# Kernel tuning notes

Hardware: AMD Instinct MI355X
Metric: run time of the kernel (lower is better)

Reference implementation:

```python
import jax, jax.numpy as jnp
import numpy as np

NN, D, H = 100000, 300, 1024   # nodes, embedding dim, hidden dim
NG, NS = 50000, 25000          # global vocab, sense vocab
B, T = 8, 128                  # batch, sequence length (state carried across all B*T steps)


def setup_inputs() -> dict:
    key = jax.random.key(0)
    ks = jax.random.split(key, 24)
    s = lambda i, shape: (jax.random.normal(ks[i], shape, jnp.float32) * 0.02)
    return {
        "x_idx": jax.random.randint(ks[0], (B, T), 0, NN),
        "X": jax.random.normal(ks[1], (NN, D), jnp.float32) * 0.1,
        "W_z_1": s(2, (D, H)), "U_z_1": s(3, (H, H)),
        "W_r_1": s(4, (D, H)), "U_r_1": s(5, (H, H)),
        "W_1": s(6, (D, H)), "b_W_1": jnp.zeros((H,), jnp.float32),
        "U_1": s(7, (H, H)), "b_U_1": jnp.zeros((H,), jnp.float32),
        "W_z_2": s(8, (H, H)), "U_z_2": s(9, (H, H)),
        "W_r_2": s(10, (H, H)), "U_r_2": s(11, (H, H)),
        "W_2": s(12, (H, H)), "b_W_2": jnp.zeros((H,), jnp.float32),
        "U_2": s(13, (H, H)), "b_U_2": jnp.zeros((H,), jnp.float32),
        "W_g": s(14, (H, NG)), "b_g": jnp.zeros((NG,), jnp.float32),
        "W_s": s(15, (H, NS)), "b_s": jnp.zeros((NS,), jnp.float32),
    }


def reference(x_idx, X, W_z_1, U_z_1, W_r_1, U_r_1, W_1, b_W_1, U_1, b_U_1,
              W_z_2, U_z_2, W_r_2, U_r_2, W_2, b_W_2, U_2, b_U_2,
              W_g, b_g, W_s, b_s):
    # The original loops over every sample of every sequence, carrying memory_h1/h2
    # across the whole batch; only X[x_indices[0]] feeds the GRU (the GAT-projected
    # neighbours are computed but never used). Dropout in eval mode = identity.
    idx = x_idx.reshape(-1)          # [S] flattened step order (seq-major per sample)
    emb = X[idx]                     # [S, D] currentword embeddings

    def step(carry, e):
        h1, h2 = carry
        z1 = jax.nn.sigmoid(e @ W_z_1 + h1 @ U_z_1)
        r1 = jax.nn.sigmoid(e @ W_r_1 + h1 @ U_r_1)
        ht1 = jnp.tanh((e @ W_1 + b_W_1) + ((r1 * h1) @ U_1 + b_U_1))
        h1n = z1 * ht1 + (1.0 - z1) * h1
        z2 = jax.nn.sigmoid(h1n @ W_z_2 + h2 @ U_z_2)
        r2 = jax.nn.sigmoid(h1n @ W_r_2 + h2 @ U_r_2)
        ht2 = jnp.tanh((h1n @ W_2 + b_W_2) + ((r2 * h2) @ U_2 + b_U_2))
        h2n = z2 * ht2 + (1.0 - z2) * h2
        return (h1n, h2n), h2n

    h0 = jnp.zeros((H,), emb.dtype)
    _, hs = jax.lax.scan(step, (h0, h0), emb)        # hs: [S, H]
    logp_g = jax.nn.log_softmax(hs @ W_g + b_g, axis=-1)   # [S, NG]
    logp_s = jax.nn.log_softmax(hs @ W_s + b_s, axis=-1)   # [S, NS]
    return logp_g, logp_s
```

## Files before the change

### kernel.cpp

```cpp
#include <hip/hip_runtime.h>

typedef __attribute__((ext_vector_type(4))) float f32x4;
typedef __attribute__((ext_vector_type(8))) __bf16 bf16x8;
typedef __attribute__((ext_vector_type(4))) unsigned short u16x4;
typedef unsigned long long ull;

#define GPAD 40
#define KEEPF(x) asm volatile("" : "+v"(x))
#define PHYS(i) ((i) + (((i) >> 6) << 2))

__device__ ull g_R[32 * 1024];
__device__ ull g_h1s[1025 * 1024];
__device__ float g_ExW[1024 * 3072];
__device__ float g_hs2[1024 * 1024];

#define H1R  0
#define RH1R (8 * 1024)
#define H2R  (16 * 1024)
#define RH2R (24 * 1024)

__device__ __forceinline__ unsigned short f2bf(float x) {
  unsigned u = __builtin_bit_cast(unsigned, x);
  u += 0x7FFFu + ((u >> 16) & 1u);
  return (unsigned short)(u >> 16);
}
__device__ __forceinline__ ull packtv(unsigned tag, float v) {
  return ((ull)tag << 32) | (ull)__builtin_bit_cast(unsigned, v);
}
__device__ __forceinline__ ull aload(const ull* p) {
  return __hip_atomic_load(p, __ATOMIC_RELAXED, __HIP_MEMORY_SCOPE_AGENT);
}
__device__ __forceinline__ void astore(ull* p, ull v) {
  __hip_atomic_store(p, v, __ATOMIC_RELAXED, __HIP_MEMORY_SCOPE_AGENT);
}
__device__ __forceinline__ float lo32(ull v) {
  return __builtin_bit_cast(float, (unsigned)v);
}

__global__ __launch_bounds__(256, 1) void fused_scan(
    const float* __restrict__ ExW,
    const float* __restrict__ Uz1, const float* __restrict__ Ur1,
    const float* __restrict__ Uw1, const float* __restrict__ bU1,
    const float* __restrict__ Wz2, const float* __restrict__ Wr2,
    const float* __restrict__ Ww2,
    const float* __restrict__ Uz2, const float* __restrict__ Ur2,
    const float* __restrict__ Uw2,
    const float* __restrict__ bW2, const float* __restrict__ bU2,
    float* __restrict__ hs2)
{
  const int tid = threadIdx.x;
  const int wv = tid >> 6, inw = tid & 63;
  __shared__ __align__(16) float h_s[1088];
  __shared__ __align__(16) float rh_s[1088];
  __shared__ __align__(16) float x_s[1088];

  if (blockIdx.x < 64) {
    const int g = blockIdx.x;
    const int rep = g & 7;
    const int c2 = inw >> 4, q = inw & 15;
    const int j = g * 16 + wv * 4 + c2;
    const int prj = g * 16 + wv * 4 + (inw >> 4);
    const bool pub = (inw & 15) < 8;
    float uz[64], ur[64], uw[64];
#pragma unroll
    for (int i = 0; i < 64; ++i) uz[i] = Uz1[(size_t)(q * 64 + i) * 1024 + j];
#pragma unroll
    for (int i = 0; i < 64; ++i) ur[i] = Ur1[(size_t)(q * 64 + i) * 1024 + j];
#pragma unroll
    for (int i = 0; i < 64; ++i) uw[i] = Uw1[(size_t)(q * 64 + i) * 1024 + j];
#pragma unroll
    for (int i = 0; i < 64; ++i) { KEEPF(uz[i]); KEEPF(ur[i]); KEEPF(uw[i]); }
    const float bu = bU1[j];

    float xz = 0.f, xr = 0.f, xw = 0.f;
    if (q == 0) { xz = ExW[j]; xr = ExW[1024 + j]; xw = ExW[2048 + j]; }

    float zreg = 0.f, hold = 0.f;
    for (int s = 0; s < 1024; ++s) {
      {
        const ull* sl = g_R + H1R + (size_t)rep * 1024 + tid * 4;
        ull a0, a1, a2, a3;
        for (;;) {
          a0 = aload(sl); a1 = aload(sl + 1); a2 = aload(sl + 2); a3 = aload(sl + 3);
          unsigned bad = ((unsigned)(a0 >> 32) ^ (unsigned)s) | ((unsigned)(a1 >> 32) ^ (unsigned)s) |
                         ((unsigned)(a2 >> 32) ^ (unsigned)s) | ((unsigned)(a3 >> 32) ^ (unsigned)s);
          if (bad == 0u) break;
          __builtin_amdgcn_s_sleep(1);
        }
        f32x4 v; v.x = lo32(a0); v.y = lo32(a1); v.z = lo32(a2); v.w = lo32(a3);
        *(f32x4*)&h_s[PHYS(tid * 4)] = v;
      }
      __syncthreads();
      if (q == 0) hold = h_s[PHYS(j)];
      float ar_ = 0.f;
      {
        const float* hp = h_s + q * 68;
#pragma unroll
        for (int i2 = 0; i2 < 16; ++i2) {
          f32x4 hv = *(const f32x4*)(hp + i2 * 4);
          ar_ = fmaf(ur[i2 * 4 + 0], hv.x, ar_); ar_ = fmaf(ur[i2 * 4 + 1], hv.y, ar_);
          ar_ = fmaf(ur[i2 * 4 + 2], hv.z, ar_); ar_ = fmaf(ur[i2 * 4 + 3], hv.w, ar_);
        }
      }
      ar_ += __shfl_xor(ar_, 1, 64); ar_ += __shfl_xor(ar_, 2, 64);
      ar_ += __shfl_xor(ar_, 4, 64); ar_ += __shfl_xor(ar_, 8, 64);
      float rhv = 0.f;
      if (q == 0) {
        float r = 1.f / (1.f + __expf(-(ar_ + xr)));
        rhv = r * hold;
      }
      {
        float pvv = __shfl(rhv, inw & 48, 64);
        ull pk = packtv((unsigned)(s + 1), pvv);
        if (pub) astore(g_R + RH1R + (size_t)(inw & 15) * 1024 + prj, pk);
      }
      float az_ = 0.f;
      {
        const float* hp = h_s + q * 68;
#pragma unroll
        for (int i2 = 0; i2 < 16; ++i2) {
          f32x4 hv = *(const f32x4*)(hp + i2 * 4);
          az_ = fmaf(uz[i2 * 4 + 0], hv.x, az_); az_ = fmaf(uz[i2 * 4 + 1], hv.y, az_);
          az_ = fmaf(uz[i2 * 4 + 2], hv.z, az_); az_ = fmaf(uz[i2 * 4 + 3], hv.w, az_);
        }
      }
      az_ += __shfl_xor(az_, 1, 64); az_ += __shfl_xor(az_, 2, 64);
      az_ += __shfl_xor(az_, 4, 64); az_ += __shfl_xor(az_, 8, 64);
      if (q == 0) zreg = 1.f / (1.f + __expf(-(az_ + xz)));
      {
        const ull* sl = g_R + RH1R + (size_t)rep * 1024 + tid * 4;
        ull a0, a1, a2, a3;
        const unsigned tg = (unsigned)(s + 1);
        for (;;) {
          a0 = aload(sl); a1 = aload(sl + 1); a2 = aload(sl + 2); a3 = aload(sl + 3);
          unsigned bad = ((unsigned)(a0 >> 32) ^ tg) | ((unsigned)(a1 >> 32) ^ tg) |
                         ((unsigned)(a2 >> 32) ^ tg) | ((unsigned)(a3 >> 32) ^ tg);
          if (bad == 0u) break;
          __builtin_amdgcn_s_sleep(1);
        }
        f32x4 v; v.x = lo32(a0); v.y = lo32(a1); v.z = lo32(a2); v.w = lo32(a3);
        *(f32x4*)&rh_s[PHYS(tid * 4)] = v;
      }
      __syncthreads();
      float aw_ = 0.f;
      {
        const float* rp = rh_s + q * 68;
#pragma unroll
        for (int i2 = 0; i2 < 16; ++i2) {
          f32x4 rv = *(const f32x4*)(rp + i2 * 4);
          aw_ = fmaf(uw[i2 * 4 + 0], rv.x, aw_); aw_ = fmaf(uw[i2 * 4 + 1], rv.y, aw_);
          aw_ = fmaf(uw[i2 * 4 + 2], rv.z, aw_); aw_ = fmaf(uw[i2 * 4 + 3], rv.w, aw_);
        }
      }
      aw_ += __shfl_xor(aw_, 1, 64); aw_ += __shfl_xor(aw_, 2, 64);
      aw_ += __shfl_xor(aw_, 4, 64); aw_ += __shfl_xor(aw_, 8, 64);
      float hn = 0.f;
      if (q == 0) {
        float ht = tanhf(aw_ + xw + bu);
        hn = zreg * ht + (1.f - zreg) * hold;
      }
      {
        float pvv = __shfl(hn, inw & 48, 64);
        ull pk = packtv((unsigned)(s + 1), pvv);
        if (pub) astore(g_R + H1R + (size_t)(inw & 15) * 1024 + prj, pk);
        if (q == 0) astore(&g_h1s[(size_t)(s + 1) * 1024 + j], pk);
      }
      float nxz = 0.f, nxr = 0.f, nxw = 0.f;
      if (q == 0 && s < 1023) {
        nxz = ExW[(s + 1) * 3072 + j];
        nxr = ExW[(s + 1) * 3072 + 1024 + j];
        nxw = ExW[(s + 1) * 3072 + 2048 + j];
      }
      xz = nxz; xr = nxr; xw = nxw;
    }
  } else {
    const int g = blockIdx.x - 64;
    const int rep = g & 7;
    const int c2 = inw >> 5, q = inw & 31;
    const int j = g * 8 + wv * 2 + c2;
    const int sb = q * 32 + ((q >> 1) << 2);
    const int prj = g * 8 + wv * 2 + (inw >> 5);
    const bool pub = (inw & 31) < 8;
    float uz[32], ur[32], uw[32], wz[32], wr[32], ww[32];
#pragma unroll
    for (int i = 0; i < 32; ++i) uz[i] = Uz2[(size_t)(q * 32 + i) * 1024 + j];
#pragma unroll
    for (int i = 0; i < 32; ++i) ur[i] = Ur2[(size_t)(q * 32 + i) * 1024 + j];
#pragma unroll
    for (int i = 0; i < 32; ++i) uw[i] = Uw2[(size_t)(q * 32 + i) * 1024 + j];
#pragma unroll
    for (int i = 0; i < 32; ++i) wz[i] = Wz2[(size_t)(q * 32 + i) * 1024 + j];
#pragma unroll
    for (int i = 0; i < 32; ++i) wr[i] = Wr2[(size_t)(q * 32 + i) * 1024 + j];
#pragma unroll
    for (int i = 0; i < 32; ++i) ww[i] = Ww2[(size_t)(q * 32 + i) * 1024 + j];
#pragma unroll
    for (int i = 0; i < 32; ++i) {
      KEEPF(uz[i]); KEEPF(ur[i]); KEEPF(uw[i]);
      KEEPF(wz[i]); KEEPF(wr[i]); KEEPF(ww[i]);
    }
    const float bu = bW2[j] + bU2[j];

    float zreg = 0.f, hold = 0.f;
    for (int s = 0; s < 1024; ++s) {
      {
        const ull* sh = g_R + H2R + (size_t)rep * 1024 + tid * 4;
        const ull* sx = g_h1s + (size_t)(s + 1) * 1024 + tid * 4;
        ull a0, a1, a2, a3, b0, b1, b2, b3;
        const unsigned tg = (unsigned)(s + 1);
        for (;;) {
          a0 = aload(sh); a1 = aload(sh + 1); a2 = aload(sh + 2); a3 = aload(sh + 3);
          b0 = aload(sx); b1 = aload(sx + 1); b2 = aload(sx + 2); b3 = aload(sx + 3);
          unsigned bad = ((unsigned)(a0 >> 32) ^ (unsigned)s) | ((unsigned)(a1 >> 32) ^ (unsigned)s) |
                         ((unsigned)(a2 >> 32) ^ (unsigned)s) | ((unsigned)(a3 >> 32) ^ (unsigned)s) |
                         ((unsigned)(b0 >> 32) ^ tg) | ((unsigned)(b1 >> 32) ^ tg) |
                         ((unsigned)(b2 >> 32) ^ tg) | ((unsigned)(b3 >> 32) ^ tg);
          if (bad == 0u) break;
          __builtin_amdgcn_s_sleep(2);
        }
        f32x4 v; v.x = lo32(a0); v.y = lo32(a1); v.z = lo32(a2); v.w = lo32(a3);
        *(f32x4*)&h_s[PHYS(tid * 4)] = v;
        f32x4 u4; u4.x = lo32(b0); u4.y = lo32(b1); u4.z = lo32(b2); u4.w = lo32(b3);
        *(f32x4*)&x_s[PHYS(tid * 4)] = u4;
      }
      __syncthreads();
      if (q == 0) hold = h_s[PHYS(j)];
      float ar_ = 0.f;
      {
        const float* hp = h_s + sb;
        const float* xp = x_s + sb;
#pragma unroll
        for (int i2 = 0; i2 < 8; ++i2) {
          f32x4 hv = *(const f32x4*)(hp + i2 * 4);
          f32x4 xv = *(const f32x4*)(xp + i2 * 4);
          ar_ = fmaf(ur[i2 * 4 + 0], hv.x, ar_); ar_ = fmaf(ur[i2 * 4 + 1], hv.y, ar_);
          ar_ = fmaf(ur[i2 * 4 + 2], hv.z, ar_); ar_ = fmaf(ur[i2 * 4 + 3], hv.w, ar_);
          ar_ = fmaf(wr[i2 * 4 + 0], xv.x, ar_); ar_ = fmaf(wr[i2 * 4 + 1], xv.y, ar_);
          ar_ = fmaf(wr[i2 * 4 + 2], xv.z, ar_); ar_ = fmaf(wr[i2 * 4 + 3], xv.w, ar_);
        }
      }
      ar_ += __shfl_xor(ar_, 1, 64); ar_ += __shfl_xor(ar_, 2, 64);
      ar_ += __shfl_xor(ar_, 4, 64); ar_ += __shfl_xor(ar_, 8, 64);
      ar_ += __shfl_xor(ar_, 16, 64);
      float rhv = 0.f;
      if (q == 0) {
        float r = 1.f / (1.f + __expf(-ar_));
        rhv = r * hold;
      }
      {
        float pvv = __shfl(rhv, inw & 32, 64);
        ull pk = packtv((unsigned)(s + 1), pvv);
        if (pub) astore(g_R + RH2R + (size_t)(inw & 31) * 1024 + prj, pk);
      }
      float az_ = 0.f;
      {
        const float* hp = h_s + sb;
        const float* xp = x_s + sb;
#pragma unroll
        for (int i2 = 0; i2 < 8; ++i2) {
          f32x4 hv = *(const f32x4*)(hp + i2 * 4);
          f32x4 xv = *(const f32x4*)(xp + i2 * 4);
          az_ = fmaf(uz[i2 * 4 + 0], hv.x, az_); az_ = fmaf(uz[i2 * 4 + 1], hv.y, az_);
          az_ = fmaf(uz[i2 * 4 + 2], hv.z, az_); az_ = fmaf(uz[i2 * 4 + 3], hv.w, az_);
          az_ = fmaf(wz[i2 * 4 + 0], xv.x, az_); az_ = fmaf(wz[i2 * 4 + 1], xv.y, az_);
          az_ = fmaf(wz[i2 * 4 + 2], xv.z, az_); az_ = fmaf(wz[i2 * 4 + 3], xv.w, az_);
        }
      }
      az_ += __shfl_xor(az_, 1, 64); az_ += __shfl_xor(az_, 2, 64);
      az_ += __shfl_xor(az_, 4, 64); az_ += __shfl_xor(az_, 8, 64);
      az_ += __shfl_xor(az_, 16, 64);
      if (q == 0) zreg = 1.f / (1.f + __expf(-az_));
      {
        const ull* sl = g_R + RH2R + (size_t)rep * 1024 + tid * 4;
        ull a0, a1, a2, a3;
        const unsigned tg = (unsigned)(s + 1);
        for (;;) {
          a0 = aload(sl); a1 = aload(sl + 1); a2 = aload(sl + 2); a3 = aload(sl + 3);
          unsigned bad = ((unsigned)(a0 >> 32) ^ tg) | ((unsigned)(a1 >> 32) ^ tg) |
                         ((unsigned)(a2 >> 32) ^ tg) | ((unsigned)(a3 >> 32) ^ tg);
          if (bad == 0u) break;
          __builtin_amdgcn_s_sleep(1);
        }
        f32x4 v; v.x = lo32(a0); v.y = lo32(a1); v.z = lo32(a2); v.w = lo32(a3);
        *(f32x4*)&rh_s[PHYS(tid * 4)] = v;
      }
      __syncthreads();
      float aw_ = 0.f;
      {
        const float* rp = rh_s + sb;
        const float* xp = x_s + sb;
#pragma unroll
        for (int i2 = 0; i2 < 8; ++i2) {
          f32x4 rv = *(const f32x4*)(rp + i2 * 4);
          f32x4 xv = *(const f32x4*)(xp + i2 * 4);
          aw_ = fmaf(uw[i2 * 4 + 0], rv.x, aw_); aw_ = fmaf(uw[i2 * 4 + 1], rv.y, aw_);
          aw_ = fmaf(uw[i2 * 4 + 2], rv.z, aw_); aw_ = fmaf(uw[i2 * 4 + 3], rv.w, aw_);
          aw_ = fmaf(ww[i2 * 4 + 0], xv.x, aw_); aw_ = fmaf(ww[i2 * 4 + 1], xv.y, aw_);
          aw_ = fmaf(ww[i2 * 4 + 2], xv.z, aw_); aw_ = fmaf(ww[i2 * 4 + 3], xv.w, aw_);
        }
      }
      aw_ += __shfl_xor(aw_, 1, 64); aw_ += __shfl_xor(aw_, 2, 64);
      aw_ += __shfl_xor(aw_, 4, 64); aw_ += __shfl_xor(aw_, 8, 64);
      aw_ += __shfl_xor(aw_, 16, 64);
      float hn = 0.f;
      if (q == 0) {
        float ht = tanhf(aw_ + bu);
        hn = zreg * ht + (1.f - zreg) * hold;
        hs2[(size_t)s * 1024 + j] = hn;
      }
      {
        float pvv = __shfl(hn, inw & 32, 64);
        ull pk = packtv((unsigned)(s + 1), pvv);
        if (pub) astore(g_R + H2R + (size_t)(inw & 31) * 1024 + prj, pk);
      }
    }
  }
}

__global__ __launch_bounds__(256, 1) void gemm_mfma(
    const float* __restrict__ A, const int* __restrict__ gidx, int lda,
    const float* __restrict__ B, int ldb,
    const float* __restrict__ bias,
    float* __restrict__ C, int ldc, int N, int K)
{
  __shared__ unsigned short As[128 * GPAD];
  __shared__ unsigned short Bs[128 * GPAD];
  const int tid = threadIdx.x;
  const int lane = tid & 63;
  const int wv = tid >> 6;
  const int wm = wv >> 1, wn = wv & 1;
  const int mbase = blockIdx.y * 128, nbase = blockIdx.x * 128;

  f32x4 acc[4][4];
#pragma unroll
  for (int i = 0; i < 4; ++i)
#pragma unroll
    for (int qq = 0; qq < 4; ++qq) acc[i][qq] = (f32x4){0.f, 0.f, 0.f, 0.f};

  const int ar = tid >> 1, ak = (tid & 1) * 16;
  const float* Arow;
  {
    int m = mbase + ar;
    long long gr = gidx ? (long long)gidx[m] : (long long)m;
    Arow = A + (size_t)gr * (size_t)lda;
  }
  const int bn = (tid >> 3) * 4;
  const int bk = (tid & 7) * 4;
  const bool nedge = (nbase + 128 > N);

  const int ksteps = (K + 31) >> 5;
  for (int ks = 0; ks < ksteps; ++ks) {
    const int k0 = ks << 5;
    __syncthreads();
    {
      float v[16];
      const int kg = k0 + ak;
      if (kg + 16 <= K) {
#pragma unroll
        for (int qq = 0; qq < 4; ++qq) {
          f32x4 t = *(const f32x4*)(Arow + kg + qq * 4);
          v[qq * 4 + 0] = t.x; v[qq * 4 + 1] = t.y; v[qq * 4 + 2] = t.z; v[qq * 4 + 3] = t.w;
        }
      } else {
#pragma unroll
        for (int i = 0; i < 16; ++i) v[i] = (kg + i < K) ? Arow[kg + i] : 0.f;
      }
#pragma unroll
      for (int qq = 0; qq < 4; ++qq) {
        u16x4 wq;
        wq.x = f2bf(v[qq * 4 + 0]); wq.y = f2bf(v[qq * 4 + 1]);
        wq.z = f2bf(v[qq * 4 + 2]); wq.w = f2bf(v[qq * 4 + 3]);
        *(u16x4*)&As[ar * GPAD + ak + qq * 4] = wq;
      }
    }
    {
      float bv[4][4];
#pragma unroll
      for (int kk = 0; kk < 4; ++kk) {
        int kglob = k0 + bk + kk;
        if (kglob < K) {
          if (!nedge) {
            f32x4 t = *(const f32x4*)(B + (size_t)kglob * (size_t)ldb + nbase + bn);
            bv[kk][0] = t.x; bv[kk][1] = t.y; bv[kk][2] = t.z; bv[kk][3] = t.w;
          } else {
#pragma unroll
            for (int nn = 0; nn < 4; ++nn) {
              int n = nbase + bn + nn;
              bv[kk][nn] = (n < N) ? B[(size_t)kglob * (size_t)ldb + n] : 0.f;
            }
          }
        } else {
          bv[kk][0] = bv[kk][1] = bv[kk][2] = bv[kk][3] = 0.f;
        }
      }
#pragma unroll
      for (int nn = 0; nn < 4; ++nn) {
        u16x4 wq;
        wq.x = f2bf(bv[0][nn]); wq.y = f2bf(bv[1][nn]);
        wq.z = f2bf(bv[2][nn]); wq.w = f2bf(bv[3][nn]);
        *(u16x4*)&Bs[(bn + nn) * GPAD + bk] = wq;
      }
    }
    __syncthreads();
    bf16x8 af[4], bfr[4];
    const int fr = lane & 15, fk = (lane >> 4) * 8;
#pragma unroll
    for (int mf = 0; mf < 4; ++mf)
      af[mf] = *(const bf16x8*)&As[(wm * 64 + mf * 16 + fr) * GPAD + fk];
#pragma unroll
    for (int nf = 0; nf < 4; ++nf)
      bfr[nf] = *(const bf16x8*)&Bs[(wn * 64 + nf * 16 + fr) * GPAD + fk];
#pragma unroll
    for (int mf = 0; mf < 4; ++mf)
#pragma unroll
      for (int nf = 0; nf < 4; ++nf)
        acc[mf][nf] = __builtin_amdgcn_mfma_f32_16x16x32_bf16(af[mf], bfr[nf], acc[mf][nf], 0, 0, 0);
  }
  const int fr = lane & 15, fq = lane >> 4;
#pragma unroll
  for (int nf = 0; nf < 4; ++nf) {
    int col = nbase + wn * 64 + nf * 16 + fr;
    if (col < N) {
      float bb = bias ? bias[col] : 0.f;
#pragma unroll
      for (int mf = 0; mf < 4; ++mf) {
        int row0 = mbase + wm * 64 + mf * 16 + fq * 4;
#pragma unroll
        for (int r = 0; r < 4; ++r)
          C[(size_t)(row0 + r) * (size_t)ldc + col] = acc[mf][nf][r] + bb;
      }
    }
  }
}

__global__ __launch_bounds__(256, 1) void logsoftmax_kernel(float* __restrict__ out) {
  const int row = blockIdx.x;
  float* p; int len;
  if (row < 1024) { p = out + (size_t)row * 50000u; len = 50000; }
  else            { p = out + 51200000ull + (size_t)(row - 1024) * 25000u; len = 25000; }
  const int tid = threadIdx.x;
  __shared__ float mred[4], sred[4];

  float m = -3.4e38f;
  for (int i = tid * 4; i < len; i += 1024) {
    f32x4 v = *(const f32x4*)(p + i);
    m = fmaxf(m, fmaxf(fmaxf(v.x, v.y), fmaxf(v.z, v.w)));
  }
#pragma unroll
  for (int off = 32; off >= 1; off >>= 1) m = fmaxf(m, __shfl_xor(m, off, 64));
  if ((tid & 63) == 0) mred[tid >> 6] = m;
  __syncthreads();
  m = fmaxf(fmaxf(mred[0], mred[1]), fmaxf(mred[2], mred[3]));

  float ssum = 0.f;
  for (int i = tid * 4; i < len; i += 1024) {
    f32x4 v = *(const f32x4*)(p + i);
    ssum += __expf(v.x - m) + __expf(v.y - m) + __expf(v.z - m) + __expf(v.w - m);
  }
#pragma unroll
  for (int off = 32; off >= 1; off >>= 1) ssum += __shfl_xor(ssum, off, 64);
  if ((tid & 63) == 0) sred[tid >> 6] = ssum;
  __syncthreads();
  const float lse = m + logf(sred[0] + sred[1] + sred[2] + sred[3]);

  for (int i = tid * 4; i < len; i += 1024) {
    f32x4 v = *(const f32x4*)(p + i);
    v.x -= lse; v.y -= lse; v.z -= lse; v.w -= lse;
    *(f32x4*)(p + i) = v;
  }
}

extern "C" void kernel_launch(void* const* d_in, const int* in_sizes, int n_in,
                              void* d_out, int out_size, void* d_ws, size_t ws_size,
                              hipStream_t stream) {
  (void)in_sizes; (void)n_in; (void)out_size; (void)d_ws; (void)ws_size;
  const int*   x_idx = (const int*)  d_in[0];
  const float* X     = (const float*)d_in[1];
  const float* W_z_1 = (const float*)d_in[2];
  const float* U_z_1 = (const float*)d_in[3];
  const float* W_r_1 = (const float*)d_in[4];
  const float* U_r_1 = (const float*)d_in[5];
  const float* W_1   = (const float*)d_in[6];
  const float* b_W_1 = (const float*)d_in[7];
  const float* U_1   = (const float*)d_in[8];
  const float* b_U_1 = (const float*)d_in[9];
  const float* W_z_2 = (const float*)d_in[10];
  const float* U_z_2 = (const float*)d_in[11];
  const float* W_r_2 = (const float*)d_in[12];
  const float* U_r_2 = (const float*)d_in[13];
  const float* W_2   = (const float*)d_in[14];
  const float* b_W_2 = (const float*)d_in[15];
  const float* U_2   = (const float*)d_in[16];
  const float* b_U_2 = (const float*)d_in[17];
  const float* W_g   = (const float*)d_in[18];
  const float* b_g   = (const float*)d_in[19];
  const float* W_s   = (const float*)d_in[20];
  const float* b_s   = (const float*)d_in[21];
  float* out = (float*)d_out;

  float *ExW, *hs2;
  ull *R, *h1s;
  hipGetSymbolAddress((void**)&ExW, HIP_SYMBOL(g_ExW));
  hipGetSymbolAddress((void**)&hs2, HIP_SYMBOL(g_hs2));
  hipGetSymbolAddress((void**)&R, HIP_SYMBOL(g_R));
  hipGetSymbolAddress((void**)&h1s, HIP_SYMBOL(g_h1s));

  const dim3 blk(256);

  hipMemsetAsync(R, 0, 32ull * 1024 * sizeof(ull), stream);
  hipMemsetAsync(h1s, 0, 1025ull * 1024 * sizeof(ull), stream);

  gemm_mfma<<<dim3(8, 8), blk, 0, stream>>>(X, x_idx, 300, W_z_1, 1024, nullptr, ExW + 0,    3072, 1024, 300);
  gemm_mfma<<<dim3(8, 8), blk, 0, stream>>>(X, x_idx, 300, W_r_1, 1024, nullptr, ExW + 1024, 3072, 1024, 300);
  gemm_mfma<<<dim3(8, 8), blk, 0, stream>>>(X, x_idx, 300, W_1,   1024, b_W_1,   ExW + 2048, 3072, 1024, 300);

  fused_scan<<<dim3(192), blk, 0, stream>>>(
      ExW, U_z_1, U_r_1, U_1, b_U_1,
      W_z_2, W_r_2, W_2, U_z_2, U_r_2, U_2, b_W_2, b_U_2, hs2);

  gemm_mfma<<<dim3(391, 8), blk, 0, stream>>>(hs2, nullptr, 1024, W_g, 50000, b_g, out,              50000, 50000, 1024);
  gemm_mfma<<<dim3(196, 8), blk, 0, stream>>>(hs2, nullptr, 1024, W_s, 25000, b_s, out + 51200000ll, 25000, 25000, 1024);
  logsoftmax_kernel<<<dim3(2048), blk, 0, stream>>>(out);
}
```

Baseline: 6.432 ms.

## Fuse output projection GEMMs into scan kernel to overlap with recurrence

```diff
diff --git a/kernel.cpp b/kernel.cpp
--- a/kernel.cpp
+++ b/kernel.cpp
@@ -11,8 +11,8 @@
 
 __device__ ull g_R[32 * 1024];
 __device__ ull g_h1s[1025 * 1024];
+__device__ ull g_h2s[1024 * 1024];
 __device__ float g_ExW[1024 * 3072];
-__device__ float g_hs2[1024 * 1024];
 
 #define H1R  0
 #define RH1R (8 * 1024)
@@ -35,6 +35,10 @@
 }
 __device__ __forceinline__ float lo32(ull v) {
   return __builtin_bit_cast(float, (unsigned)v);
+}
+__device__ __forceinline__ unsigned tagbad4(ull a0, ull a1, ull a2, ull a3, unsigned tg) {
+  return ((unsigned)(a0 >> 32) ^ tg) | ((unsigned)(a1 >> 32) ^ tg) |
+         ((unsigned)(a2 >> 32) ^ tg) | ((unsigned)(a3 >> 32) ^ tg);
 }
 
 __global__ __launch_bounds__(256, 1) void fused_scan(
@@ -46,15 +50,17 @@
     const float* __restrict__ Uz2, const float* __restrict__ Ur2,
     const float* __restrict__ Uw2,
     const float* __restrict__ bW2, const float* __restrict__ bU2,
-    float* __restrict__ hs2)
+    const float* __restrict__ Wg, const float* __restrict__ bg,
+    const float* __restrict__ Ws, const float* __restrict__ bs,
+    float* __restrict__ out)
 {
   const int tid = threadIdx.x;
   const int wv = tid >> 6, inw = tid & 63;
-  __shared__ __align__(16) float h_s[1088];
-  __shared__ __align__(16) float rh_s[1088];
-  __shared__ __align__(16) float x_s[1088];
+  __shared__ __align__(16) char smem[20480];
 
   if (blockIdx.x < 64) {
+    float* h_s = (float*)smem;
+    float* rh_s = h_s + 1088;
     const int g = blockIdx.x;
     const int rep = g & 7;
     const int c2 = inw >> 4, q = inw & 15;
@@ -82,9 +88,7 @@
         ull a0, a1, a2, a3;
         for (;;) {
           a0 = aload(sl); a1 = aload(sl + 1); a2 = aload(sl + 2); a3 = aload(sl + 3);
-          unsigned bad = ((unsigned)(a0 >> 32) ^ (unsigned)s) | ((unsigned)(a1 >> 32) ^ (unsigned)s) |
-                         ((unsigned)(a2 >> 32) ^ (unsigned)s) | ((unsigned)(a3 >> 32) ^ (unsigned)s);
-          if (bad == 0u) break;
+          if (!tagbad4(a0, a1, a2, a3, (unsigned)s)) break;
           __builtin_amdgcn_s_sleep(1);
         }
         f32x4 v; v.x = lo32(a0); v.y = lo32(a1); v.z = lo32(a2); v.w = lo32(a3);
@@ -133,9 +137,7 @@
         const unsigned tg = (unsigned)(s + 1);
         for (;;) {
           a0 = aload(sl); a1 = aload(sl + 1); a2 = aload(sl + 2); a3 = aload(sl + 3);
-          unsigned bad = ((unsigned)(a0 >> 32) ^ tg) | ((unsigned)(a1 >> 32) ^ tg) |
-                         ((unsigned)(a2 >> 32) ^ tg) | ((unsigned)(a3 >> 32) ^ tg);
-          if (bad == 0u) break;
+          if (!tagbad4(a0, a1, a2, a3, tg)) break;
           __builtin_amdgcn_s_sleep(1);
         }
         f32x4 v; v.x = lo32(a0); v.y = lo32(a1); v.z = lo32(a2); v.w = lo32(a3);
@@ -173,7 +175,10 @@
       }
       xz = nxz; xr = nxr; xw = nxw;
     }
-  } else {
+  } else if (blockIdx.x < 192) {
+    float* h_s = (float*)smem;
+    float* rh_s = h_s + 1088;
+    float* x_s = rh_s + 1088;
     const int g = blockIdx.x - 64;
     const int rep = g & 7;
     const int c2 = inw >> 5, q = inw & 31;
@@ -211,10 +216,7 @@
         for (;;) {
           a0 = aload(sh); a1 = aload(sh + 1); a2 = aload(sh + 2); a3 = aload(sh + 3);
           b0 = aload(sx); b1 = aload(sx + 1); b2 = aload(sx + 2); b3 = aload(sx + 3);
-          unsigned bad = ((unsigned)(a0 >> 32) ^ (unsigned)s) | ((unsigned)(a1 >> 32) ^ (unsigned)s) |
-                         ((unsigned)(a2 >> 32) ^ (unsigned)s) | ((unsigned)(a3 >> 32) ^ (unsigned)s) |
-                         ((unsigned)(b0 >> 32) ^ tg) | ((unsigned)(b1 >> 32) ^ tg) |
-                         ((unsigned)(b2 >> 32) ^ tg) | ((unsigned)(b3 >> 32) ^ tg);
+          unsigned bad = tagbad4(a0, a1, a2, a3, (unsigned)s) | tagbad4(b0, b1, b2, b3, tg);
           if (bad == 0u) break;
           __builtin_amdgcn_s_sleep(2);
         }
@@ -276,9 +278,7 @@
         const unsigned tg = (unsigned)(s + 1);
         for (;;) {
           a0 = aload(sl); a1 = aload(sl + 1); a2 = aload(sl + 2); a3 = aload(sl + 3);
-          unsigned bad = ((unsigned)(a0 >> 32) ^ tg) | ((unsigned)(a1 >> 32) ^ tg) |
-                         ((unsigned)(a2 >> 32) ^ tg) | ((unsigned)(a3 >> 32) ^ tg);
-          if (bad == 0u) break;
+          if (!tagbad4(a0, a1, a2, a3, tg)) break;
           __builtin_amdgcn_s_sleep(1);
         }
         f32x4 v; v.x = lo32(a0); v.y = lo32(a1); v.z = lo32(a2); v.w = lo32(a3);
@@ -306,13 +306,134 @@
       if (q == 0) {
         float ht = tanhf(aw_ + bu);
         hn = zreg * ht + (1.f - zreg) * hold;
-        hs2[(size_t)s * 1024 + j] = hn;
+        astore(&g_h2s[(size_t)s * 1024 + j], packtv((unsigned)(s + 1), hn));
       }
       {
         float pvv = __shfl(hn, inw & 32, 64);
         ull pk = packtv((unsigned)(s + 1), pvv);
         if (pub) astore(g_R + H2R + (size_t)(inw & 31) * 1024 + prj, pk);
       }
+    }
+  } else {
+    unsigned short* As = (unsigned short*)smem;
+    unsigned short* Bs = As + 128 * GPAD;
+    const int wid = blockIdx.x - 192;
+    const int lane = tid & 63;
+    const int wm = wv >> 1, wn = wv & 1;
+    const int ar = tid >> 1, ak = (tid & 1) * 16;
+    const int bn = (tid >> 3) * 4, bk = (tid & 7) * 4;
+    const int TILES = 587 * 8;
+
+    for (int t5 = wid; t5 < TILES; t5 += 64) {
+      const int rt = t5 / 587, u = t5 % 587;
+      const float* B; const float* bias; float* C; int N; int ct;
+      if (u < 391) { B = Wg; bias = bg; C = out; N = 50000; ct = u; }
+      else         { B = Ws; bias = bs; C = out + 51200000ll; N = 25000; ct = u - 391; }
+      const int mbase = rt * 128, nbase = ct * 128;
+      const bool nedge = (nbase + 128 > N);
+
+      {
+        const ull* gp = g_h2s + (size_t)(mbase + 127) * 1024 + tid * 4;
+        const unsigned tg = (unsigned)(mbase + 128);
+        for (;;) {
+          ull a0 = aload(gp), a1 = aload(gp + 1), a2 = aload(gp + 2), a3 = aload(gp + 3);
+          if (!tagbad4(a0, a1, a2, a3, tg)) break;
+          __builtin_amdgcn_s_sleep(32);
+        }
+      }
+      __syncthreads();
+
+      f32x4 acc[4][4];
+#pragma unroll
+      for (int i = 0; i < 4; ++i)
+#pragma unroll
+        for (int qq = 0; qq < 4; ++qq) acc[i][qq] = (f32x4){0.f, 0.f, 0.f, 0.f};
+
+      for (int ks = 0; ks < 32; ++ks) {
+        const int k0 = ks << 5;
+        __syncthreads();
+        {
+          const ull* ap = g_h2s + (size_t)(mbase + ar) * 1024 + k0 + ak;
+          const unsigned tg = (unsigned)(mbase + ar + 1);
+          float v[16];
+          for (;;) {
+            unsigned bad = 0u;
+#pragma unroll
+            for (int i = 0; i < 16; ++i) {
+              ull w = aload(ap + i);
+              bad |= ((unsigned)(w >> 32)) ^ tg;
+              v[i] = lo32(w);
+            }
+            if (bad == 0u) break;
+            __builtin_amdgcn_s_sleep(16);
+          }
+#pragma unroll
+          for (int qq = 0; qq < 4; ++qq) {
+            u16x4 wq;
+            wq.x = f2bf(v[qq * 4 + 0]); wq.y = f2bf(v[qq * 4 + 1]);
+            wq.z = f2bf(v[qq * 4 + 2]); wq.w = f2bf(v[qq * 4 + 3]);
+            *(u16x4*)&As[ar * GPAD + ak + qq * 4] = wq;
+          }
+        }
+        {
+          float bv[4][4];
+#pragma unroll
+          for (int kk = 0; kk < 4; ++kk) {
+            const int kglob = k0 + bk + kk;
+            if (!nedge) {
+              f32x4 t4 = __builtin_nontemporal_load(
+                  (const f32x4*)(B + (size_t)kglob * (size_t)N + nbase + bn));
+              bv[kk][0] = t4.x; bv[kk][1] = t4.y; bv[kk][2] = t4.z; bv[kk][3] = t4.w;
+            } else {
+#pragma unroll
+              for (int nn = 0; nn < 4; ++nn) {
+                int n = nbase + bn + nn;
+                bv[kk][nn] = (n < N)
+                    ? __builtin_nontemporal_load(B + (size_t)kglob * (size_t)N + n) : 0.f;
+              }
+            }
+          }
+#pragma unroll
+          for (int nn = 0; nn < 4; ++nn) {
+            u16x4 wq;
+            wq.x = f2bf(bv[0][nn]); wq.y = f2bf(bv[1][nn]);
+            wq.z = f2bf(bv[2][nn]); wq.w = f2bf(bv[3][nn]);
+            *(u16x4*)&Bs[(bn + nn) * GPAD + bk] = wq;
+          }
+        }
+        __syncthreads();
+        bf16x8 af[4], bfr[4];
+        const int fr = lane & 15, fk = (lane >> 4) * 8;
+#pragma unroll
+        for (int mf = 0; mf < 4; ++mf)
+          af[mf] = *(const bf16x8*)&As[(wm * 64 + mf * 16 + fr) * GPAD + fk];
+#pragma unroll
+        for (int nf = 0; nf < 4; ++nf)
+          bfr[nf] = *(const bf16x8*)&Bs[(wn * 64 + nf * 16 + fr) * GPAD + fk];
+#pragma unroll
+        for (int mf = 0; mf < 4; ++mf)
+#pragma unroll
+          for (int nf = 0; nf < 4; ++nf)
+            acc[mf][nf] = __builtin_amdgcn_mfma_f32_16x16x32_bf16(af[mf], bfr[nf], acc[mf][nf], 0, 0, 0);
+      }
+      {
+        const int fr = lane & 15, fq = lane >> 4;
+#pragma unroll
+        for (int nf = 0; nf < 4; ++nf) {
+          int col = nbase + wn * 64 + nf * 16 + fr;
+          if (col < N) {
+            float bb = bias[col];
+#pragma unroll
+            for (int mf = 0; mf < 4; ++mf) {
+              int row0 = mbase + wm * 64 + mf * 16 + fq * 4;
+#pragma unroll
+              for (int r = 0; r < 4; ++r)
+                C[(size_t)(row0 + r) * (size_t)N + col] = acc[mf][nf][r] + bb;
+            }
+          }
+        }
+      }
+      __syncthreads();
     }
   }
 }
@@ -498,27 +619,27 @@
   const float* b_s   = (const float*)d_in[21];
   float* out = (float*)d_out;
 
-  float *ExW, *hs2;
-  ull *R, *h1s;
+  float* ExW;
+  ull *R, *h1s, *h2s;
   hipGetSymbolAddress((void**)&ExW, HIP_SYMBOL(g_ExW));
-  hipGetSymbolAddress((void**)&hs2, HIP_SYMBOL(g_hs2));
   hipGetSymbolAddress((void**)&R, HIP_SYMBOL(g_R));
   hipGetSymbolAddress((void**)&h1s, HIP_SYMBOL(g_h1s));
+  hipGetSymbolAddress((void**)&h2s, HIP_SYMBOL(g_h2s));
 
   const dim3 blk(256);
 
   hipMemsetAsync(R, 0, 32ull * 1024 * sizeof(ull), stream);
   hipMemsetAsync(h1s, 0, 1025ull * 1024 * sizeof(ull), stream);
+  hipMemsetAsync(h2s, 0, 1024ull * 1024 * sizeof(ull), stream);
 
   gemm_mfma<<<dim3(8, 8), blk, 0, stream>>>(X, x_idx, 300, W_z_1, 1024, nullptr, ExW + 0,    3072, 1024, 300);
   gemm_mfma<<<dim3(8, 8), blk, 0, stream>>>(X, x_idx, 300, W_r_1, 1024, nullptr, ExW + 1024, 3072, 1024, 300);
   gemm_mfma<<<dim3(8, 8), blk, 0, stream>>>(X, x_idx, 300, W_1,   1024, b_W_1,   ExW + 2048, 3072, 1024, 300);
 
-  fused_scan<<<dim3(192), blk, 0, stream>>>(
+  fused_scan<<<dim3(256), blk, 0, stream>>>(
       ExW, U_z_1, U_r_1, U_1, b_U_1,
-      W_z_2, W_r_2, W_2, U_z_2, U_r_2, U_2, b_W_2, b_U_2, hs2);
-
-  gemm_mfma<<<dim3(391, 8), blk, 0, stream>>>(hs2, nullptr, 1024, W_g, 50000, b_g, out,              50000, 50000, 1024);
-  gemm_mfma<<<dim3(196, 8), blk, 0, stream>>>(hs2, nullptr, 1024, W_s, 25000, b_s, out + 51200000ll, 25000, 25000, 1024);
+      W_z_2, W_r_2, W_2, U_z_2, U_r_2, U_2, b_W_2, b_U_2,
+      W_g, b_g, W_s, b_s, out);
+
   logsoftmax_kernel<<<dim3(2048), blk, 0, stream>>>(out);
 }
```

After: 11.04 ms. +71.7%, slower.
